# Kernel optimization log

Hardware: AMD Instinct MI355X
Metric: run time of the kernel (lower is better)

The kernel has to match this reference:

```python
import jax, jax.numpy as jnp
import numpy as np


def setup_inputs() -> dict:
    key = jax.random.key(0)
    kx, ky = jax.random.split(key)
    x = jax.random.normal(kx, (8192, 256), dtype=jnp.float32)
    y = jax.random.normal(ky, (8192, 256), dtype=jnp.float32)
    return {"x": x, "y": y, "gamma": 1.0}


def reference(x, y, gamma):
    # RBF kernel: exp(-gamma * ||x_i - y_j||^2), computed without the
    x_sq = jnp.sum(x * x, axis=-1)            # [N]
    y_sq = jnp.sum(y * y, axis=-1)            # [M]
    cross = jnp.einsum('nd,md->nm', x, y)     # [N, M]
    sq_dist = x_sq[:, None] + y_sq[None, :] - 2.0 * cross
    sq_dist = jnp.maximum(sq_dist, 0.0)       # guard tiny negatives from fp error
    return jnp.exp(-gamma * sq_dist)
```

## Files before the change

### kernel.cpp

```cpp
#include <hip/hip_runtime.h>

#define NR 8192
#define DK 256
#define BM 128
#define BN 128
#define BK 64

typedef __bf16 bf16x8 __attribute__((ext_vector_type(8)));
typedef float f32x4 __attribute__((ext_vector_type(4)));
typedef unsigned short ushort_t;
typedef unsigned int uint_t;

__device__ __forceinline__ ushort_t f2bf(float f) {
  uint_t u = __float_as_uint(f);
  u += 0x7fffu + ((u >> 16) & 1u);
  return (ushort_t)(u >> 16);
}

__global__ __launch_bounds__(256) void prep_kernel(
    const float* __restrict__ x, const float* __restrict__ y,
    ushort_t* __restrict__ xb, ushort_t* __restrict__ yb,
    float* __restrict__ xsq, float* __restrict__ ysq) {
  int row = blockIdx.x * 4 + (threadIdx.x >> 6);
  int lane = threadIdx.x & 63;
  const float* src; ushort_t* dst; float* sq; int r;
  if (row < NR) { src = x; dst = xb; sq = xsq; r = row; }
  else          { src = y; dst = yb; sq = ysq; r = row - NR; }
  float4 v = ((const float4*)(src + (size_t)r * DK))[lane];
  float s = v.x * v.x + v.y * v.y + v.z * v.z + v.w * v.w;
  ushort4 o;
  o.x = f2bf(v.x); o.y = f2bf(v.y); o.z = f2bf(v.z); o.w = f2bf(v.w);
  ((ushort4*)(dst + (size_t)r * DK))[lane] = o;
#pragma unroll
  for (int off = 32; off; off >>= 1) s += __shfl_xor(s, off, 64);
  if (lane == 0) sq[r] = s;
}

__global__ __launch_bounds__(256) void rbf_gemm(
    const ushort_t* __restrict__ xb, const ushort_t* __restrict__ yb,
    const float* __restrict__ xsq, const float* __restrict__ ysq,
    const float* __restrict__ gptr, float* __restrict__ out) {
  __shared__ ushort_t lds[2 * BM * BK];
  ushort_t* ldsA = lds;
  ushort_t* ldsB = lds + BM * BK;

  const int t = threadIdx.x;
  const int wid = t >> 6, lane = t & 63;
  const int wm = wid >> 1, wn = wid & 1;
  const int tm = blockIdx.x, tn = blockIdx.y;

  f32x4 acc[4][4];
#pragma unroll
  for (int i = 0; i < 4; ++i)
#pragma unroll
    for (int j = 0; j < 4; ++j)
      acc[i][j] = (f32x4){0.f, 0.f, 0.f, 0.f};

  const int c_row = t >> 3;
  const int c_col = (t & 7) * 8;

  for (int kt = 0; kt < DK / BK; ++kt) {
    const int k0 = kt * BK;
#pragma unroll
    for (int s = 0; s < 4; ++s) {
      const ushort_t* gA = xb + (size_t)(tm * BM + s * 32 + c_row) * DK + k0 + c_col;
      const ushort_t* gB = yb + (size_t)(tn * BN + s * 32 + c_row) * DK + k0 + c_col;
      char* lA = (char*)ldsA + s * 4096 + wid * 1024;
      char* lB = (char*)ldsB + s * 4096 + wid * 1024;
      __builtin_amdgcn_global_load_lds(
          (const __attribute__((address_space(1))) void*)gA,
          (__attribute__((address_space(3))) void*)lA, 16, 0, 0);
      __builtin_amdgcn_global_load_lds(
          (const __attribute__((address_space(1))) void*)gB,
          (__attribute__((address_space(3))) void*)lB, 16, 0, 0);
    }
    __syncthreads();

    {
      const int fr = lane & 15, fk = lane >> 4;
      bf16x8 af[4][2], bfr[4][2];
#pragma unroll
      for (int i = 0; i < 4; ++i) {
#pragma unroll
        for (int kk = 0; kk < 2; ++kk) {
          const int rowA = wm * 64 + i * 16 + fr;
          af[i][kk] = *(const bf16x8*)((const char*)ldsA + rowA * 128 + kk * 64 + fk * 16);
          const int rowB = wn * 64 + i * 16 + fr;
          bfr[i][kk] = *(const bf16x8*)((const char*)ldsB + rowB * 128 + kk * 64 + fk * 16);
        }
      }
#pragma unroll
      for (int i = 0; i < 4; ++i)
#pragma unroll
        for (int j = 0; j < 4; ++j)
#pragma unroll
          for (int kk = 0; kk < 2; ++kk)
            acc[i][j] = __builtin_amdgcn_mfma_f32_16x16x32_bf16(
                af[i][kk], bfr[j][kk], acc[i][j], 0, 0, 0);
    }
    __syncthreads();
  }

  const float gamma = *gptr;
  const int fr = lane & 15, fq = lane >> 4;
  const int rowbase = tm * BM + wm * 64;
  const int colbase = tn * BN + wn * 64;
#pragma unroll
  for (int i = 0; i < 4; ++i) {
    float xs[4];
#pragma unroll
    for (int r = 0; r < 4; ++r)
      xs[r] = xsq[rowbase + i * 16 + fq * 4 + r];
#pragma unroll
    for (int j = 0; j < 4; ++j) {
      const int gcol = colbase + j * 16 + fr;
      const float yv = ysq[gcol];
#pragma unroll
      for (int r = 0; r < 4; ++r) {
        const int grow = rowbase + i * 16 + fq * 4 + r;
        float d = xs[r] + yv - 2.0f * acc[i][j][r];
        d = fmaxf(d, 0.0f);
        out[(size_t)grow * NR + gcol] = __expf(-gamma * d);
      }
    }
  }
}

extern "C" void kernel_launch(void* const* d_in, const int* in_sizes, int n_in,
                              void* d_out, int out_size, void* d_ws, size_t ws_size,
                              hipStream_t stream) {
  const float* x = (const float*)d_in[0];
  const float* y = (const float*)d_in[1];
  const float* gamma = (const float*)d_in[2];
  float* out = (float*)d_out;
  char* ws = (char*)d_ws;
  ushort_t* xb = (ushort_t*)ws;
  ushort_t* yb = (ushort_t*)(ws + (size_t)NR * DK * 2);
  float* xsq = (float*)(ws + (size_t)NR * DK * 4);
  float* ysq = (float*)(ws + (size_t)NR * DK * 4 + (size_t)NR * 4);

  prep_kernel<<<dim3((2 * NR) / 4), dim3(256), 0, stream>>>(x, y, xb, yb, xsq, ysq);
  rbf_gemm<<<dim3(NR / BM, NR / BN), dim3(256), 0, stream>>>(xb, yb, xsq, ysq, gamma, out);
}
```

Baseline: 303.5 us.

## Load MFMA operands directly from global memory and swizzle block order

Drops the LDS staging and the per-k-tile barriers, so each wave loads its bf16 A and B fragments straight from global memory into registers across a fully unrolled K loop. It also remaps the flat block index so that consecutive workgroups are spread across the tile grid, which changes L2 locality and the write pattern. The aim is to remove LDS traffic and synchronisation from a GEMM with short K (256) whose run time is dominated by the output write. The cost is that each wave re-reads operand rows other waves also read, relying on L1/L2 caching, and the fragment loads are strided 16-byte accesses.

```diff
diff --git a/kernel.cpp b/kernel.cpp
--- a/kernel.cpp
+++ b/kernel.cpp
@@ -4,7 +4,6 @@
 #define DK 256
 #define BM 128
 #define BN 128
-#define BK 64
 
 typedef __bf16 bf16x8 __attribute__((ext_vector_type(8)));
 typedef float f32x4 __attribute__((ext_vector_type(4)));
@@ -40,14 +39,16 @@
     const ushort_t* __restrict__ xb, const ushort_t* __restrict__ yb,
     const float* __restrict__ xsq, const float* __restrict__ ysq,
     const float* __restrict__ gptr, float* __restrict__ out) {
-  __shared__ ushort_t lds[2 * BM * BK];
-  ushort_t* ldsA = lds;
-  ushort_t* ldsB = lds + BM * BK;
-
   const int t = threadIdx.x;
   const int wid = t >> 6, lane = t & 63;
   const int wm = wid >> 1, wn = wid & 1;
-  const int tm = blockIdx.x, tn = blockIdx.y;
+
+  const int flat = blockIdx.y * gridDim.x + blockIdx.x;
+  const int swz = (flat & 7) * 512 + (flat >> 3);
+  const int tm = swz & 63;
+  const int tn = swz >> 6;
+
+  const int fr = lane & 15, fk = lane >> 4;
 
   f32x4 acc[4][4];
 #pragma unroll
@@ -56,53 +57,28 @@
     for (int j = 0; j < 4; ++j)
       acc[i][j] = (f32x4){0.f, 0.f, 0.f, 0.f};
 
-  const int c_row = t >> 3;
-  const int c_col = (t & 7) * 8;
+  const ushort_t* Abase = xb + (size_t)(tm * BM + wm * 64 + fr) * DK + fk * 8;
+  const ushort_t* Bbase = yb + (size_t)(tn * BN + wn * 64 + fr) * DK + fk * 8;
 
-  for (int kt = 0; kt < DK / BK; ++kt) {
-    const int k0 = kt * BK;
 #pragma unroll
-    for (int s = 0; s < 4; ++s) {
-      const ushort_t* gA = xb + (size_t)(tm * BM + s * 32 + c_row) * DK + k0 + c_col;
-      const ushort_t* gB = yb + (size_t)(tn * BN + s * 32 + c_row) * DK + k0 + c_col;
-      char* lA = (char*)ldsA + s * 4096 + wid * 1024;
-      char* lB = (char*)ldsB + s * 4096 + wid * 1024;
-      __builtin_amdgcn_global_load_lds(
-          (const __attribute__((address_space(1))) void*)gA,
-          (__attribute__((address_space(3))) void*)lA, 16, 0, 0);
-      __builtin_amdgcn_global_load_lds(
-          (const __attribute__((address_space(1))) void*)gB,
-          (__attribute__((address_space(3))) void*)lB, 16, 0, 0);
-    }
-    __syncthreads();
-
-    {
-      const int fr = lane & 15, fk = lane >> 4;
-      bf16x8 af[4][2], bfr[4][2];
+  for (int ks = 0; ks < 8; ++ks) {
+    bf16x8 a[4], b[4];
 #pragma unroll
-      for (int i = 0; i < 4; ++i) {
+    for (int i = 0; i < 4; ++i)
+      a[i] = *(const bf16x8*)(Abase + (size_t)i * 16 * DK + ks * 32);
 #pragma unroll
-        for (int kk = 0; kk < 2; ++kk) {
-          const int rowA = wm * 64 + i * 16 + fr;
-          af[i][kk] = *(const bf16x8*)((const char*)ldsA + rowA * 128 + kk * 64 + fk * 16);
-          const int rowB = wn * 64 + i * 16 + fr;
-          bfr[i][kk] = *(const bf16x8*)((const char*)ldsB + rowB * 128 + kk * 64 + fk * 16);
-        }
-      }
+    for (int j = 0; j < 4; ++j)
+      b[j] = *(const bf16x8*)(Bbase + (size_t)j * 16 * DK + ks * 32);
 #pragma unroll
-      for (int i = 0; i < 4; ++i)
+    for (int i = 0; i < 4; ++i)
 #pragma unroll
-        for (int j = 0; j < 4; ++j)
-#pragma unroll
-          for (int kk = 0; kk < 2; ++kk)
-            acc[i][j] = __builtin_amdgcn_mfma_f32_16x16x32_bf16(
-                af[i][kk], bfr[j][kk], acc[i][j], 0, 0, 0);
-    }
-    __syncthreads();
+      for (int j = 0; j < 4; ++j)
+        acc[i][j] = __builtin_amdgcn_mfma_f32_16x16x32_bf16(
+            a[i], b[j], acc[i][j], 0, 0, 0);
   }
 
   const float gamma = *gptr;
-  const int fr = lane & 15, fq = lane >> 4;
+  const int fq = lane >> 4;
   const int rowbase = tm * BM + wm * 64;
   const int colbase = tn * BN + wn * 64;
 #pragma unroll
```

Measured after the change: 400.8 us. +32.0%, slower.
